# Optimization experiments

Measured on AMD Instinct MI355X. Metric: run time of the kernel, lower is better.

## Reference

```python
import jax, jax.numpy as jnp
import numpy as np

NUM_USER, NUM_ITEM, NUM_TIME = 200000, 100000, 5000
P, Q, R = 32, 32, 32
N = 131072


def _xavier(key, shape):
    fan_in, fan_out = shape[0], int(np.prod(shape[1:]))
    limit = float(np.sqrt(6.0 / (fan_in + fan_out)))
    return jax.random.uniform(key, shape, dtype=jnp.float32, minval=-limit, maxval=limit)


def setup_inputs() -> dict:
    key = jax.random.key(0)
    k1, k2, k3, k4, k5, k6, k7 = jax.random.split(key, 7)
    return {
        "i_input": jax.random.randint(k1, (N,), 0, NUM_USER),
        "j_input": jax.random.randint(k2, (N,), 0, NUM_ITEM),
        "k_input": jax.random.randint(k3, (N,), 0, NUM_TIME),
        "user_embeddings": _xavier(k4, (NUM_USER, P)),
        "item_embeddings": _xavier(k5, (NUM_ITEM, Q)),
        "time_embeddings": _xavier(k6, (NUM_TIME, R)),
        "core_tensor": _xavier(k7, (P, Q, R)),
    }


def reference(i_input, j_input, k_input, user_embeddings, item_embeddings,
              time_embeddings, core_tensor):
    # Gather per-sample embeddings: [n,p], [n,q], [n,r]
    i_embeds = user_embeddings[i_input]
    j_embeds = item_embeddings[j_input]
    k_embeds = time_embeddings[k_input]
    # Fused Tucker contraction: never materialize the (n,p,q,r) outer product.
    # Mathematically identical to einsum('np,nq,nr,pqr->n', ...).
    t = jnp.einsum('np,pqr->nqr', i_embeds, core_tensor)  # [n,q,r]
    t = jnp.einsum('nqr,nq->nr', t, j_embeds)             # [n,r]
    return jnp.einsum('nr,nr->n', t, k_embeds)            # [n]
```

## Files before the change

kernel.cpp:

```cpp
#include <hip/hip_runtime.h>


#define BIN_CAP 128

__global__ __launch_bounds__(256) void build_H(const float* __restrict__ G,
                                               const float* __restrict__ W,
                                               float* __restrict__ H,
                                               int num_time) {
    const int pq4 = threadIdx.x;
    const int kbase = blockIdx.x * 8;

    float acc[8][4];
#pragma unroll
    for (int kk = 0; kk < 8; ++kk)
#pragma unroll
        for (int i = 0; i < 4; ++i) acc[kk][i] = 0.f;

#pragma unroll
    for (int r4 = 0; r4 < 8; ++r4) {
        float4 g[4];
#pragma unroll
        for (int i = 0; i < 4; ++i)
            g[i] = *(const float4*)(G + (size_t)(pq4 * 4 + i) * 32 + r4 * 4);
#pragma unroll
        for (int kk = 0; kk < 8; ++kk) {
            int k = kbase + kk;
            int kc = (k < num_time) ? k : (num_time - 1);
            float4 w = *(const float4*)(W + (size_t)kc * 32 + r4 * 4);
#pragma unroll
            for (int i = 0; i < 4; ++i)
                acc[kk][i] += g[i].x * w.x + g[i].y * w.y + g[i].z * w.z + g[i].w * w.w;
        }
    }

#pragma unroll
    for (int kk = 0; kk < 8; ++kk) {
        int k = kbase + kk;
        if (k < num_time) {
            float4 o = make_float4(acc[kk][0], acc[kk][1], acc[kk][2], acc[kk][3]);
            *(float4*)(H + (size_t)k * 1024 + pq4 * 4) = o;
        }
    }
}

__global__ __launch_bounds__(256) void scatter_k(const int* __restrict__ K,
                                                 const int* __restrict__ I,
                                                 const int* __restrict__ J,
                                                 int* __restrict__ counts,
                                                 int4* __restrict__ bins,
                                                 int* __restrict__ ovf_cnt,
                                                 int4* __restrict__ ovf,
                                                 int n) {
    for (int idx = blockIdx.x * blockDim.x + threadIdx.x; idx < n;
         idx += gridDim.x * blockDim.x) {
        int k = K[idx];
        int4 rec = make_int4(idx, I[idx], J[idx], k);
        int pos = atomicAdd(&counts[k], 1);
        if (pos < BIN_CAP) {
            bins[(size_t)k * BIN_CAP + pos] = rec;
        } else {
            int o = atomicAdd(ovf_cnt, 1);
            ovf[o] = rec;
        }
    }
}

__global__ __launch_bounds__(256) void tucker_eval_grouped(
        const float* __restrict__ U, const float* __restrict__ V,
        const float* __restrict__ H, const int* __restrict__ counts,
        const int4* __restrict__ bins, float* __restrict__ out,
        int num_time) {
    __shared__ float4 Hs4[4][256];
    const int wave = threadIdx.x >> 6;
    const int lane = threadIdx.x & 63;
    const int k = blockIdx.x * 4 + wave;
    const int qq = lane & 7;
    const int s8 = lane >> 3;

    int m = 0;
    if (k < num_time) {
        const float4* __restrict__ Hrow4 = (const float4*)(H + (size_t)k * 1024);
#pragma unroll
        for (int c = 0; c < 4; ++c)
            Hs4[wave][lane + 64 * c] = Hrow4[lane + 64 * c];
        m = counts[k];
        m = (m < BIN_CAP) ? m : BIN_CAP;
    }
    __syncthreads();
    if (k >= num_time || m == 0) return;

    const int iters = (m + 7) >> 3;
    const float4* __restrict__ Hw = Hs4[wave];

    for (int t = 0; t < iters; ++t) {
        const int s = t * 8 + s8;
        if (s < m) {
            int4 rec = bins[(size_t)k * BIN_CAP + s];
            const float4* __restrict__ Ur = (const float4*)(U + (size_t)rec.y * 32);
            float4 u[8];
#pragma unroll
            for (int p4 = 0; p4 < 8; ++p4) u[p4] = Ur[p4];
            float4 v4 = ((const float4*)(V + (size_t)rec.z * 32))[qq];

            float4 acc = make_float4(0.f, 0.f, 0.f, 0.f);
#pragma unroll
            for (int p4 = 0; p4 < 8; ++p4) {
                float4 h;
                h = Hw[(p4 * 4 + 0) * 8 + qq];
                acc.x += u[p4].x * h.x; acc.y += u[p4].x * h.y;
                acc.z += u[p4].x * h.z; acc.w += u[p4].x * h.w;
                h = Hw[(p4 * 4 + 1) * 8 + qq];
                acc.x += u[p4].y * h.x; acc.y += u[p4].y * h.y;
                acc.z += u[p4].y * h.z; acc.w += u[p4].y * h.w;
                h = Hw[(p4 * 4 + 2) * 8 + qq];
                acc.x += u[p4].z * h.x; acc.y += u[p4].z * h.y;
                acc.z += u[p4].z * h.z; acc.w += u[p4].z * h.w;
                h = Hw[(p4 * 4 + 3) * 8 + qq];
                acc.x += u[p4].w * h.x; acc.y += u[p4].w * h.y;
                acc.z += u[p4].w * h.z; acc.w += u[p4].w * h.w;
            }
            float sd = acc.x * v4.x + acc.y * v4.y + acc.z * v4.z + acc.w * v4.w;
            sd += __shfl_xor(sd, 1, 64);
            sd += __shfl_xor(sd, 2, 64);
            sd += __shfl_xor(sd, 4, 64);
            if (qq == 0) out[rec.x] = sd;
        }
    }
}

__global__ __launch_bounds__(256) void tucker_eval_overflow(
        const float* __restrict__ U, const float* __restrict__ V,
        const float* __restrict__ H, const int* __restrict__ ovf_cnt,
        const int4* __restrict__ ovf, float* __restrict__ out) {
    const int gwave = (int)((blockIdx.x * (unsigned)blockDim.x + threadIdx.x) >> 6);
    const int nwaves = (int)((gridDim.x * (unsigned)blockDim.x) >> 6);
    const int lane = threadIdx.x & 63;
    const int qq = lane & 7;
    const int pg = lane >> 3;
    const int cnt = *ovf_cnt;

    for (int s = gwave; s < cnt; s += nwaves) {
        int4 rec = ovf[s];
        const float4* __restrict__ Hrow = (const float4*)(H + (size_t)rec.w * 1024);
        const float* __restrict__ Ur = U + (size_t)rec.y * 32;

        float4 acc = make_float4(0.f, 0.f, 0.f, 0.f);
#pragma unroll
        for (int it = 0; it < 4; ++it) {
            float4 h = Hrow[lane + it * 64];
            float up = Ur[pg + it * 8];
            acc.x += up * h.x; acc.y += up * h.y;
            acc.z += up * h.z; acc.w += up * h.w;
        }
#pragma unroll
        for (int off = 8; off < 64; off <<= 1) {
            acc.x += __shfl_xor(acc.x, off, 64);
            acc.y += __shfl_xor(acc.y, off, 64);
            acc.z += __shfl_xor(acc.z, off, 64);
            acc.w += __shfl_xor(acc.w, off, 64);
        }
        float4 v4 = ((const float4*)(V + (size_t)rec.z * 32))[qq];
        float sd = acc.x * v4.x + acc.y * v4.y + acc.z * v4.z + acc.w * v4.w;
        sd += __shfl_xor(sd, 1, 64);
        sd += __shfl_xor(sd, 2, 64);
        sd += __shfl_xor(sd, 4, 64);
        if (lane == 0) out[rec.x] = sd;
    }
}

__global__ __launch_bounds__(256) void tucker_eval(const int* __restrict__ I,
                                                   const int* __restrict__ J,
                                                   const int* __restrict__ K,
                                                   const float* __restrict__ U,
                                                   const float* __restrict__ V,
                                                   const float* __restrict__ H,
                                                   float* __restrict__ out,
                                                   int n_samples) {
    const int wave = (int)((blockIdx.x * (unsigned)blockDim.x + threadIdx.x) >> 6);
    const int lane = threadIdx.x & 63;
    if (wave >= n_samples) return;
    const int i = I[wave];
    const int j = J[wave];
    const int k = K[wave];
    const int qq = lane & 7;
    const int pg = lane >> 3;
    const float4* __restrict__ Hrow = (const float4*)(H + (size_t)k * 1024);
    const float* __restrict__ Urow = U + (size_t)i * 32;
    float4 acc = make_float4(0.f, 0.f, 0.f, 0.f);
#pragma unroll
    for (int it = 0; it < 4; ++it) {
        float4 h = Hrow[lane + it * 64];
        float up = Urow[pg + it * 8];
        acc.x += up * h.x; acc.y += up * h.y;
        acc.z += up * h.z; acc.w += up * h.w;
    }
#pragma unroll
    for (int off = 8; off < 64; off <<= 1) {
        acc.x += __shfl_xor(acc.x, off, 64);
        acc.y += __shfl_xor(acc.y, off, 64);
        acc.z += __shfl_xor(acc.z, off, 64);
        acc.w += __shfl_xor(acc.w, off, 64);
    }
    float4 v4 = ((const float4*)(V + (size_t)j * 32))[qq];
    float s = acc.x * v4.x + acc.y * v4.y + acc.z * v4.z + acc.w * v4.w;
    s += __shfl_xor(s, 1, 64);
    s += __shfl_xor(s, 2, 64);
    s += __shfl_xor(s, 4, 64);
    if (lane == 0) out[wave] = s;
}

__global__ __launch_bounds__(256) void tucker_direct(const int* __restrict__ I,
                                                     const int* __restrict__ J,
                                                     const int* __restrict__ K,
                                                     const float* __restrict__ U,
                                                     const float* __restrict__ V,
                                                     const float* __restrict__ W,
                                                     const float* __restrict__ G,
                                                     float* __restrict__ out,
                                                     int n_samples) {
    __shared__ float Gc[4 * 32 * 32];
    const int n = blockIdx.x * blockDim.x + threadIdx.x;
    const bool active = (n < n_samples);
    int i = 0, j = 0, k = 0;
    if (active) { i = I[n]; j = J[n]; k = K[n]; }
    float4 w4[8];
#pragma unroll
    for (int r4 = 0; r4 < 8; ++r4)
        w4[r4] = ((const float4*)(W + (size_t)k * 32))[r4];
    float v[32];
#pragma unroll
    for (int q4 = 0; q4 < 8; ++q4) {
        float4 t = ((const float4*)(V + (size_t)j * 32))[q4];
        v[q4 * 4 + 0] = t.x; v[q4 * 4 + 1] = t.y;
        v[q4 * 4 + 2] = t.z; v[q4 * 4 + 3] = t.w;
    }
    const float* __restrict__ Urow = U + (size_t)i * 32;
    float acc = 0.f;
    for (int c = 0; c < 8; ++c) {
        __syncthreads();
#pragma unroll
        for (int t = 0; t < 4; ++t) {
            int idx = threadIdx.x + t * 256;
            ((float4*)Gc)[idx] = ((const float4*)(G + (size_t)c * 4096))[idx];
        }
        __syncthreads();
        for (int pp = 0; pp < 4; ++pp) {
            float up = Urow[c * 4 + pp];
#pragma unroll
            for (int q = 0; q < 32; ++q) {
                float t0 = 0.f;
#pragma unroll
                for (int r4 = 0; r4 < 8; ++r4) {
                    float4 g = ((const float4*)Gc)[pp * 256 + q * 8 + r4];
                    t0 += g.x * w4[r4].x + g.y * w4[r4].y + g.z * w4[r4].z + g.w * w4[r4].w;
                }
                acc += up * v[q] * t0;
            }
        }
    }
    if (active) out[n] = acc;
}

extern "C" void kernel_launch(void* const* d_in, const int* in_sizes, int n_in,
                              void* d_out, int out_size, void* d_ws, size_t ws_size,
                              hipStream_t stream) {
    const int*   I = (const int*)d_in[0];
    const int*   J = (const int*)d_in[1];
    const int*   K = (const int*)d_in[2];
    const float* U = (const float*)d_in[3];
    const float* V = (const float*)d_in[4];
    const float* W = (const float*)d_in[5];
    const float* G = (const float*)d_in[6];
    float* out = (float*)d_out;

    const int n_samples = in_sizes[0];
    const int num_time = in_sizes[5] / 32;

    const size_t h_bytes = (size_t)num_time * 1024 * sizeof(float);
    const size_t z_bytes = (size_t)(num_time + 1) * sizeof(int);
    const size_t z_pad = (z_bytes + 15) & ~(size_t)15;
    const size_t bins_bytes = (size_t)num_time * BIN_CAP * sizeof(int4);
    const size_t ovf_bytes = (size_t)n_samples * sizeof(int4);
    const size_t need_full = h_bytes + z_pad + bins_bytes + ovf_bytes;

    if (ws_size >= need_full) {
        float* H       = (float*)d_ws;
        int*   counts  = (int*)((char*)d_ws + h_bytes);
        int*   ovf_cnt = counts + num_time;
        int4*  bins    = (int4*)((char*)d_ws + h_bytes + z_pad);
        int4*  ovf     = (int4*)((char*)d_ws + h_bytes + z_pad + bins_bytes);

        hipMemsetAsync(counts, 0, z_bytes, stream);
        scatter_k<<<512, 256, 0, stream>>>(K, I, J, counts, bins, ovf_cnt, ovf,
                                           n_samples);
        build_H<<<(num_time + 7) / 8, 256, 0, stream>>>(G, W, H, num_time);
        tucker_eval_grouped<<<(num_time + 3) / 4, 256, 0, stream>>>(
            U, V, H, counts, bins, out, num_time);
        tucker_eval_overflow<<<64, 256, 0, stream>>>(U, V, H, ovf_cnt, ovf, out);
    } else if (ws_size >= h_bytes) {
        float* H = (float*)d_ws;
        build_H<<<(num_time + 7) / 8, 256, 0, stream>>>(G, W, H, num_time);
        const long long total_threads = (long long)n_samples * 64;
        tucker_eval<<<(int)((total_threads + 255) / 256), 256, 0, stream>>>(
            I, J, K, U, V, H, out, n_samples);
    } else {
        tucker_direct<<<(n_samples + 255) / 256, 256, 0, stream>>>(
            I, J, K, U, V, W, G, out, n_samples);
    }
}
```

Baseline: 135.5 us.

## Fuse H build with scatter, fold overflow into grouped eval, prefetch records

Merges the build_H and scatter kernels into one launch whose blocks split by index, so the two independent preparation stages run concurrently. It also folds the overflow-evaluation pass into the tail of the grouped evaluation kernel, which removes a launch, and prefetches the next bin record one iteration ahead to hide its load latency. This cuts launch count and idle gaps between small kernels. The cost is that every grouped block now reads the overflow counter, and the fused kernel's block mix may be scheduled unevenly.

```diff
diff --git a/kernel.cpp b/kernel.cpp
--- a/kernel.cpp
+++ b/kernel.cpp
@@ -3,12 +3,12 @@
 
 #define BIN_CAP 128
 
-__global__ __launch_bounds__(256) void build_H(const float* __restrict__ G,
-                                               const float* __restrict__ W,
-                                               float* __restrict__ H,
-                                               int num_time) {
+__device__ __forceinline__ void build_H_body(const float* __restrict__ G,
+                                             const float* __restrict__ W,
+                                             float* __restrict__ H,
+                                             int num_time, int bblk) {
     const int pq4 = threadIdx.x;
-    const int kbase = blockIdx.x * 8;
+    const int kbase = bblk * 8;
 
     float acc[8][4];
 #pragma unroll
@@ -43,16 +43,15 @@
     }
 }
 
-__global__ __launch_bounds__(256) void scatter_k(const int* __restrict__ K,
-                                                 const int* __restrict__ I,
-                                                 const int* __restrict__ J,
-                                                 int* __restrict__ counts,
-                                                 int4* __restrict__ bins,
-                                                 int* __restrict__ ovf_cnt,
-                                                 int4* __restrict__ ovf,
-                                                 int n) {
-    for (int idx = blockIdx.x * blockDim.x + threadIdx.x; idx < n;
-         idx += gridDim.x * blockDim.x) {
+__device__ __forceinline__ void scatter_body(const int* __restrict__ K,
+                                             const int* __restrict__ I,
+                                             const int* __restrict__ J,
+                                             int* __restrict__ counts,
+                                             int4* __restrict__ bins,
+                                             int* __restrict__ ovf_cnt,
+                                             int4* __restrict__ ovf,
+                                             int n, int sblk, int nsblk) {
+    for (int idx = sblk * 256 + (int)threadIdx.x; idx < n; idx += nsblk * 256) {
         int k = K[idx];
         int4 rec = make_int4(idx, I[idx], J[idx], k);
         int pos = atomicAdd(&counts[k], 1);
@@ -65,11 +64,35 @@
     }
 }
 
+__global__ __launch_bounds__(256) void fused_prepare(
+        const float* __restrict__ G, const float* __restrict__ W,
+        float* __restrict__ H,
+        const int* __restrict__ K, const int* __restrict__ I,
+        const int* __restrict__ J, int* __restrict__ counts,
+        int4* __restrict__ bins, int* __restrict__ ovf_cnt,
+        int4* __restrict__ ovf, int n, int num_time,
+        int nbuild, int nscatter) {
+    const int b = blockIdx.x;
+    if (b < nbuild) {
+        build_H_body(G, W, H, num_time, b);
+    } else {
+        scatter_body(K, I, J, counts, bins, ovf_cnt, ovf, n, b - nbuild, nscatter);
+    }
+}
+
+__global__ __launch_bounds__(256) void build_H(const float* __restrict__ G,
+                                               const float* __restrict__ W,
+                                               float* __restrict__ H,
+                                               int num_time) {
+    build_H_body(G, W, H, num_time, blockIdx.x);
+}
+
 __global__ __launch_bounds__(256) void tucker_eval_grouped(
         const float* __restrict__ U, const float* __restrict__ V,
         const float* __restrict__ H, const int* __restrict__ counts,
         const int4* __restrict__ bins, float* __restrict__ out,
-        int num_time) {
+        int num_time, const int* __restrict__ ovf_cnt,
+        const int4* __restrict__ ovf) {
     __shared__ float4 Hs4[4][256];
     const int wave = threadIdx.x >> 6;
     const int lane = threadIdx.x & 63;
@@ -87,20 +110,26 @@
         m = (m < BIN_CAP) ? m : BIN_CAP;
     }
     __syncthreads();
-    if (k >= num_time || m == 0) return;
-
-    const int iters = (m + 7) >> 3;
-    const float4* __restrict__ Hw = Hs4[wave];
-
-    for (int t = 0; t < iters; ++t) {
-        const int s = t * 8 + s8;
-        if (s < m) {
-            int4 rec = bins[(size_t)k * BIN_CAP + s];
+
+    if (k < num_time && m > 0) {
+        const int iters = (m + 7) >> 3;
+        const float4* __restrict__ Hw = Hs4[wave];
+        const int4* __restrict__ bbase = bins + (size_t)k * BIN_CAP;
+
+        int sc = (s8 < m) ? s8 : (m - 1);
+        int4 rec = bbase[sc];
+
+        for (int t = 0; t < iters; ++t) {
+            const int s = t * 8 + s8;
             const float4* __restrict__ Ur = (const float4*)(U + (size_t)rec.y * 32);
             float4 u[8];
 #pragma unroll
             for (int p4 = 0; p4 < 8; ++p4) u[p4] = Ur[p4];
             float4 v4 = ((const float4*)(V + (size_t)rec.z * 32))[qq];
+
+            int sn = s + 8;
+            sn = (sn < m) ? sn : (m - 1);
+            int4 rec_n = bbase[sn];
 
             float4 acc = make_float4(0.f, 0.f, 0.f, 0.f);
 #pragma unroll
@@ -123,48 +152,43 @@
             sd += __shfl_xor(sd, 1, 64);
             sd += __shfl_xor(sd, 2, 64);
             sd += __shfl_xor(sd, 4, 64);
-            if (qq == 0) out[rec.x] = sd;
-        }
-    }
-}
-
-__global__ __launch_bounds__(256) void tucker_eval_overflow(
-        const float* __restrict__ U, const float* __restrict__ V,
-        const float* __restrict__ H, const int* __restrict__ ovf_cnt,
-        const int4* __restrict__ ovf, float* __restrict__ out) {
-    const int gwave = (int)((blockIdx.x * (unsigned)blockDim.x + threadIdx.x) >> 6);
-    const int nwaves = (int)((gridDim.x * (unsigned)blockDim.x) >> 6);
-    const int lane = threadIdx.x & 63;
-    const int qq = lane & 7;
-    const int pg = lane >> 3;
+            if (s < m && qq == 0) out[rec.x] = sd;
+            rec = rec_n;
+        }
+    }
+
     const int cnt = *ovf_cnt;
-
-    for (int s = gwave; s < cnt; s += nwaves) {
-        int4 rec = ovf[s];
-        const float4* __restrict__ Hrow = (const float4*)(H + (size_t)rec.w * 1024);
-        const float* __restrict__ Ur = U + (size_t)rec.y * 32;
-
-        float4 acc = make_float4(0.f, 0.f, 0.f, 0.f);
-#pragma unroll
-        for (int it = 0; it < 4; ++it) {
-            float4 h = Hrow[lane + it * 64];
-            float up = Ur[pg + it * 8];
-            acc.x += up * h.x; acc.y += up * h.y;
-            acc.z += up * h.z; acc.w += up * h.w;
-        }
-#pragma unroll
-        for (int off = 8; off < 64; off <<= 1) {
-            acc.x += __shfl_xor(acc.x, off, 64);
-            acc.y += __shfl_xor(acc.y, off, 64);
-            acc.z += __shfl_xor(acc.z, off, 64);
-            acc.w += __shfl_xor(acc.w, off, 64);
-        }
-        float4 v4 = ((const float4*)(V + (size_t)rec.z * 32))[qq];
-        float sd = acc.x * v4.x + acc.y * v4.y + acc.z * v4.z + acc.w * v4.w;
-        sd += __shfl_xor(sd, 1, 64);
-        sd += __shfl_xor(sd, 2, 64);
-        sd += __shfl_xor(sd, 4, 64);
-        if (lane == 0) out[rec.x] = sd;
+    if (cnt > 0) {
+        const int gwave = (int)blockIdx.x * 4 + wave;
+        const int nw = (int)gridDim.x * 4;
+        const int pg = lane >> 3;
+        for (int s = gwave; s < cnt; s += nw) {
+            int4 rec = ovf[s];
+            const float4* __restrict__ Hrow = (const float4*)(H + (size_t)rec.w * 1024);
+            const float* __restrict__ Ur = U + (size_t)rec.y * 32;
+
+            float4 acc = make_float4(0.f, 0.f, 0.f, 0.f);
+#pragma unroll
+            for (int it = 0; it < 4; ++it) {
+                float4 h = Hrow[lane + it * 64];
+                float up = Ur[pg + it * 8];
+                acc.x += up * h.x; acc.y += up * h.y;
+                acc.z += up * h.z; acc.w += up * h.w;
+            }
+#pragma unroll
+            for (int off = 8; off < 64; off <<= 1) {
+                acc.x += __shfl_xor(acc.x, off, 64);
+                acc.y += __shfl_xor(acc.y, off, 64);
+                acc.z += __shfl_xor(acc.z, off, 64);
+                acc.w += __shfl_xor(acc.w, off, 64);
+            }
+            float4 v4 = ((const float4*)(V + (size_t)rec.z * 32))[qq];
+            float sd = acc.x * v4.x + acc.y * v4.y + acc.z * v4.z + acc.w * v4.w;
+            sd += __shfl_xor(sd, 1, 64);
+            sd += __shfl_xor(sd, 2, 64);
+            sd += __shfl_xor(sd, 4, 64);
+            if (lane == 0) out[rec.x] = sd;
+        }
     }
 }
 
@@ -290,13 +314,15 @@
         int4*  bins    = (int4*)((char*)d_ws + h_bytes + z_pad);
         int4*  ovf     = (int4*)((char*)d_ws + h_bytes + z_pad + bins_bytes);
 
+        const int nbuild = (num_time + 7) / 8;
+        const int nscatter = 512;
+
         hipMemsetAsync(counts, 0, z_bytes, stream);
-        scatter_k<<<512, 256, 0, stream>>>(K, I, J, counts, bins, ovf_cnt, ovf,
-                                           n_samples);
-        build_H<<<(num_time + 7) / 8, 256, 0, stream>>>(G, W, H, num_time);
+        fused_prepare<<<nbuild + nscatter, 256, 0, stream>>>(
+            G, W, H, K, I, J, counts, bins, ovf_cnt, ovf,
+            n_samples, num_time, nbuild, nscatter);
         tucker_eval_grouped<<<(num_time + 3) / 4, 256, 0, stream>>>(
-            U, V, H, counts, bins, out, num_time);
-        tucker_eval_overflow<<<64, 256, 0, stream>>>(U, V, H, ovf_cnt, ovf, out);
+            U, V, H, counts, bins, out, num_time, ovf_cnt, ovf);
     } else if (ws_size >= h_bytes) {
         float* H = (float*)d_ws;
         build_H<<<(num_time + 7) / 8, 256, 0, stream>>>(G, W, H, num_time);
```

After: 135.5 us. Within noise of the previous version (-0.0%).
